# Performance work log

Hardware: AMD Instinct MI355X
Metric: run time of the kernel (lower is better)

Reference implementation:

```python
import jax, jax.numpy as jnp
import numpy as np

B, P, T = 32, 196, 32           # batch, num pixels (14*14), seq_len
E, H, A, V = 512, 512, 256, 30000  # embed, hidden, attention, vocab
FEAT = 2048

def _ln(x, g, b, eps=1e-5):
    m = jnp.mean(x, -1, keepdims=True)
    v = jnp.mean((x - m) ** 2, -1, keepdims=True)
    return (x - m) / jnp.sqrt(v + eps) * g + b

def setup_inputs() -> dict:
    key = jax.random.key(0)
    ks = iter(jax.random.split(key, 32))
    def rn(shape, s=0.05):
        return (jax.random.normal(next(ks), shape, dtype=jnp.float32) * s)
    inp = {
        'features': jax.random.normal(next(ks), (B, P, FEAT), dtype=jnp.float32),
        'captions': jax.random.randint(next(ks), (B, T), 0, V),
        # feature adapter Linear(2048->E) + LayerNorm
        'Wad': rn((E, FEAT)), 'bad': jnp.zeros((E,), jnp.float32),
        'g_ad': jnp.ones((E,), jnp.float32), 'b_ad': jnp.zeros((E,), jnp.float32),
        # additive attention
        'We': rn((A, E)), 'be': jnp.zeros((A,), jnp.float32),
        'Wd': rn((A, H)), 'bd': jnp.zeros((A,), jnp.float32),
        'Wf': rn((1, A)), 'bf': jnp.zeros((1,), jnp.float32),
        # embedding table (uniform(-0.1,0.1) as in torch init)
        'emb': jax.random.uniform(next(ks), (V, E), jnp.float32, -0.1, 0.1),
        # LSTM layer 0: input 2E, layer 1: input H; gates order i,f,g,o; forget bias 1
        'W_ih0': rn((4 * H, 2 * E)), 'W_hh0': rn((4 * H, H)),
        'b_ih0': jnp.concatenate([jnp.zeros(H), jnp.ones(H), jnp.zeros(2 * H)]).astype(jnp.float32),
        'b_hh0': jnp.zeros((4 * H,), jnp.float32),
        'W_ih1': rn((4 * H, H)), 'W_hh1': rn((4 * H, H)),
        'b_ih1': jnp.concatenate([jnp.zeros(H), jnp.ones(H), jnp.zeros(2 * H)]).astype(jnp.float32),
        'b_hh1': jnp.zeros((4 * H,), jnp.float32),
        # output head
        'W1': rn((H // 2, H)), 'b1': jnp.zeros((H // 2,), jnp.float32),
        'g1': jnp.ones((H // 2,), jnp.float32), 'bb1': jnp.zeros((H // 2,), jnp.float32),
        'W2': rn((V, H // 2)), 'b2': jnp.zeros((V,), jnp.float32),
    }
    return inp

def reference(features, captions, Wad, bad, g_ad, b_ad, We, be, Wd, bd, Wf, bf,
              emb, W_ih0, W_hh0, b_ih0, b_hh0, W_ih1, W_hh1, b_ih1, b_hh1,
              W1, b1, g1, bb1, W2, b2):
    # feature adapter (dropout = identity in eval)
    enc = _ln(jax.nn.relu(features @ Wad.T + bad), g_ad, b_ad)   # [B,P,E]
    att1 = enc @ We.T + be                                        # [B,P,A] (same every step)
    embs = emb[captions]                                          # [B,T,E]

    def lstm_cell(x, h, c, Wih, Whh, bih, bhh):
        gates = x @ Wih.T + bih + h @ Whh.T + bhh                 # [B,4H]
        i, f, g, o = jnp.split(gates, 4, axis=1)
        c_n = jax.nn.sigmoid(f) * c + jax.nn.sigmoid(i) * jnp.tanh(g)
        h_n = jax.nn.sigmoid(o) * jnp.tanh(c_n)
        return h_n, c_n

    def step(carry, emb_t):
        h, c = carry                                              # each [2,B,H]
        # additive attention against top-layer hidden state
        att2 = h[1] @ Wd.T + bd                                   # [B,A]
        e = (jax.nn.relu(att1 + att2[:, None, :]) @ Wf.T + bf)[..., 0]  # [B,P]
        alpha = jax.nn.softmax(e, axis=1)                         # (max-subtract is folded in)
        ctx = jnp.einsum('bp,bpe->be', alpha, enc)                # [B,E]
        x = jnp.concatenate([emb_t, ctx], axis=1)                 # [B,2E]
        h0, c0 = lstm_cell(x,  h[0], c[0], W_ih0, W_hh0, b_ih0, b_hh0)
        h1, c1 = lstm_cell(h0, h[1], c[1], W_ih1, W_hh1, b_ih1, b_hh1)
        out = jax.nn.relu(_ln(h1 @ W1.T + b1, g1, bb1))
        out = jnp.clip(out @ W2.T + b2, -10.0, 10.0)              # [B,V]
        return (jnp.stack([h0, h1]), jnp.stack([c0, c1])), out

    h0 = jnp.zeros((2, B, H), jnp.float32)
    c0 = jnp.zeros((2, B, H), jnp.float32)
    _, outs = jax.lax.scan(step, (h0, c0), jnp.swapaxes(embs, 0, 1))
    return jnp.swapaxes(outs, 0, 1)                               # [B,T,V]
```

## Files before the change

### kernel.cpp

```cpp
#include <hip/hip_runtime.h>

#define B_ 32
#define P_ 196
#define T_ 32
#define E_ 512
#define H_ 512
#define A_ 256
#define V_ 30000
#define FEAT_ 2048

typedef unsigned short u16;
typedef __attribute__((ext_vector_type(8))) short bf16x8;
typedef __attribute__((ext_vector_type(4))) float fx4;

#define MFMA16 __builtin_amdgcn_mfma_f32_16x16x32_bf16

__device__ __forceinline__ u16 f2b(float f){
  unsigned u = __builtin_bit_cast(unsigned, f);
  u += 0x7FFFu + ((u >> 16) & 1u);
  return (u16)(u >> 16);
}
__device__ __forceinline__ float b2f(u16 h){
  unsigned u = ((unsigned)h) << 16;
  return __builtin_bit_cast(float, u);
}
__device__ __forceinline__ float sigm(float x){ return 1.f/(1.f + __expf(-x)); }

__global__ void k_convert(const float* __restrict__ src, u16* __restrict__ dst, int n8){
  int i = blockIdx.x*256 + threadIdx.x;
  if (i >= n8) return;
  const float4* s = (const float4*)src + (size_t)i*2;
  float4 a = s[0], b = s[1];
  ushort4* d = (ushort4*)dst + (size_t)i*2;
  d[0] = make_ushort4(f2b(a.x), f2b(a.y), f2b(a.z), f2b(a.w));
  d[1] = make_ushort4(f2b(b.x), f2b(b.y), f2b(b.z), f2b(b.w));
}

__global__ void k_gather(const float* __restrict__ emb, const int* __restrict__ cap,
                         u16* __restrict__ dst){
  int r = blockIdx.x, l = threadIdx.x;
  int t = r >> 5, b = r & 31;
  int c = cap[b*T_ + t];
  const float4* s = (const float4*)(emb + (size_t)c*E_) + l*2;
  float4 a = s[0], bb = s[1];
  ushort4* d = (ushort4*)(dst + (size_t)r*E_) + l*2;
  d[0] = make_ushort4(f2b(a.x), f2b(a.y), f2b(a.z), f2b(a.w));
  d[1] = make_ushort4(f2b(bb.x), f2b(bb.y), f2b(bb.z), f2b(bb.w));
}

__global__ void k_pack_wd2(const float* __restrict__ Wd, unsigned* __restrict__ dst){
  int i = blockIdx.x*256 + threadIdx.x;
  if (i >= 256*256) return;
  int n = i & 255, kp = i >> 8;
  unsigned lo = f2b(Wd[n*512 + 2*kp]);
  unsigned hi = f2b(Wd[n*512 + 2*kp + 1]);
  dst[i] = lo | (hi << 16);
}

__global__ void k_pack_g0(const float* __restrict__ Wih, const float* __restrict__ Whh,
                          u16* __restrict__ dst){
  int eid = blockIdx.x*256 + threadIdx.x;
  if (eid >= 6144*512) return;
  int j = eid & 7, l = (eid >> 3) & 63, frag = eid >> 9;
  int ks = frag % 12; int rest = frag / 12;
  int kw = rest & 3, q = (rest >> 2) & 3, s = rest >> 4;
  int n = q*512 + s*16 + (l & 15);
  int k = kw*384 + ks*32 + ((l >> 4) << 3) + j;
  float v = (k < 1024) ? Wih[(size_t)n*1024 + k] : Whh[(size_t)n*512 + (k - 1024)];
  dst[eid] = f2b(v);
}

__global__ void k_pack_w1p(const float* __restrict__ Wih, const float* __restrict__ Whh,
                           u16* __restrict__ dst){
  int eid = blockIdx.x*256 + threadIdx.x;
  if (eid >= 32*128*512) return;
  int j = eid & 7, l = (eid >> 3) & 63, f = eid >> 9;
  int nf = f & 127, s = f >> 7;
  int np = nf*16 + (l & 15);
  int k = ((l >> 4) << 3) + j;
  int orig = ((np >> 4) & 3)*512 + (np >> 6)*16 + (np & 15);
  float v = (k < 16) ? Wih[(size_t)orig*512 + s*16 + k]
                     : Whh[(size_t)orig*512 + s*16 + (k - 16)];
  dst[eid] = f2b(v);
}

__global__ void k_bias_pack(const float* __restrict__ bih, const float* __restrict__ bhh,
                            float* __restrict__ dst){
  int n = blockIdx.x*256 + threadIdx.x;
  if (n >= 2048) return;
  int c = n & 15, q = (n >> 4) & 3, s = n >> 6;
  int orig = q*512 + s*16 + c;
  dst[n] = bih[orig] + bhh[orig];
}

template<int MODE, int BM, int BN>
__launch_bounds__(256)
__global__ void k_gemm(const u16* __restrict__ A, const u16* __restrict__ W,
                       const float* __restrict__ bias, float* __restrict__ outF,
                       u16* __restrict__ outB, int M, int N, int K){
  constexpr int NI = BN/32, MI = BM/32;
  __shared__ __align__(16) u16 As[BM][40];
  __shared__ __align__(16) u16 Bs[BN][40];
  int tid = threadIdx.x;
  int l = tid & 63, w = tid >> 6;
  int wr = w >> 1, wc = w & 1;
  int m0 = blockIdx.y * BM, n0 = blockIdx.x * BN;
  fx4 acc[MI][NI];
  #pragma unroll
  for (int i=0;i<MI;i++)
    #pragma unroll
    for (int j=0;j<NI;j++) acc[i][j] = (fx4){0.f,0.f,0.f,0.f};
  int r = tid >> 2, seg = tid & 3;
  int lr = l & 15, lg = l >> 4;
  for (int k0 = 0; k0 < K; k0 += 32){
    #pragma unroll
    for (int pa=0; pa<BM/64; pa++)
      *(uint4*)&As[r+pa*64][seg*8] = *(const uint4*)(A + (size_t)(m0+r+pa*64)*K + k0 + seg*8);
    uint4 z = {0u,0u,0u,0u};
    #pragma unroll
    for (int pb=0; pb<BN/64; pb++){
      int rb = n0 + r + pb*64;
      *(uint4*)&Bs[r+pb*64][seg*8] = (rb < N) ? *(const uint4*)(W + (size_t)rb*K + k0 + seg*8) : z;
    }
    __syncthreads();
    bf16x8 av[MI], bv[NI];
    #pragma unroll
    for (int mi=0; mi<MI; mi++) av[mi] = *(const bf16x8*)&As[wr*(BM/2) + mi*16 + lr][lg*8];
    #pragma unroll
    for (int ni=0; ni<NI; ni++) bv[ni] = *(const bf16x8*)&Bs[wc*(BN/2) + ni*16 + lr][lg*8];
    #pragma unroll
    for (int mi=0; mi<MI; mi++)
      #pragma unroll
      for (int ni=0; ni<NI; ni++)
        acc[mi][ni] = MFMA16(av[mi], bv[ni], acc[mi][ni], 0, 0, 0);
    __syncthreads();
  }
  #pragma unroll
  for (int mi=0; mi<MI; mi++)
    #pragma unroll
    for (int ni=0; ni<NI; ni++){
      int col = n0 + wc*(BN/2) + ni*16 + lr;
      if (col >= N) continue;
      float bvs = bias[col];
      #pragma unroll
      for (int reg=0; reg<4; reg++){
        int rowm = m0 + wr*(BM/2) + mi*16 + lg*4 + reg;
        float v = acc[mi][ni][reg] + bvs;
        if (MODE == 0){ v = fmaxf(v, 0.f); outB[(size_t)rowm*N + col] = f2b(v); }
        else if (MODE == 1){ outB[(size_t)rowm*N + col] = f2b(v); }
        else if (MODE == 2){ outF[(size_t)rowm*N + col] = v; }
        else {
          v = fminf(fmaxf(v, -10.f), 10.f);
          outF[(size_t)rowm*V_ + col] = v;
        }
      }
    }
}

__global__ void k_ln1(const u16* __restrict__ pre, const float* __restrict__ g,
                      const float* __restrict__ bt, u16* __restrict__ enc){
  int row = blockIdx.x; int l = threadIdx.x;
  bf16x8 vv = *(const bf16x8*)(pre + (size_t)row*E_ + l*8);
  float x[8]; float s = 0.f;
  #pragma unroll
  for (int i=0;i<8;i++){ x[i] = b2f((u16)vv[i]); s += x[i]; }
  #pragma unroll
  for (int off=32; off; off>>=1) s += __shfl_xor(s, off, 64);
  float mean = s * (1.f/512.f);
  float vs = 0.f;
  #pragma unroll
  for (int i=0;i<8;i++){ float d = x[i]-mean; vs += d*d; }
  #pragma unroll
  for (int off=32; off; off>>=1) vs += __shfl_xor(vs, off, 64);
  float inv = rsqrtf(vs*(1.f/512.f) + 1e-5f);
  int c0 = l*8;
  u16 o[8];
  #pragma unroll
  for (int i=0;i<8;i++) o[i] = f2b((x[i]-mean)*inv*g[c0+i] + bt[c0+i]);
  ushort4* d = (ushort4*)(enc + (size_t)row*E_ + c0);
  d[0] = make_ushort4(o[0],o[1],o[2],o[3]);
  d[1] = make_ushort4(o[4],o[5],o[6],o[7]);
}

__global__ void k_ln2(const float* __restrict__ pre1, const float* __restrict__ g,
                      const float* __restrict__ bb, u16* __restrict__ hid){
  int row = blockIdx.x; int l = threadIdx.x;
  float4 v = *(const float4*)(pre1 + (size_t)row*256 + l*4);
  float x[4] = {v.x, v.y, v.z, v.w};
  float s = x[0]+x[1]+x[2]+x[3];
  #pragma unroll
  for (int off=32; off; off>>=1) s += __shfl_xor(s, off, 64);
  float mean = s * (1.f/256.f);
  float vs = 0.f;
  #pragma unroll
  for (int i=0;i<4;i++){ float d = x[i]-mean; vs += d*d; }
  #pragma unroll
  for (int off=32; off; off>>=1) vs += __shfl_xor(vs, off, 64);
  float inv = rsqrtf(vs*(1.f/256.f) + 1e-5f);
  int c0 = l*4;
  u16 o[4];
  #pragma unroll
  for (int i=0;i<4;i++) o[i] = f2b(fmaxf((x[i]-mean)*inv*g[c0+i] + bb[c0+i], 0.f));
  *(ushort4*)(hid + (size_t)row*256 + c0) = make_ushort4(o[0],o[1],o[2],o[3]);
}

__launch_bounds__(1024)
__global__ void k_ly(const float* __restrict__ part1, const float* __restrict__ bias1p,
                     float* __restrict__ c1buf, u16* __restrict__ h1all,
                     const unsigned* __restrict__ Wd2, const float* __restrict__ bd,
                     const u16* __restrict__ att1b, const u16* __restrict__ enc16,
                     const float* __restrict__ Wf, const float* __restrict__ bfp,
                     const u16* __restrict__ embs, u16* __restrict__ xh0cur, int t){
  int b = blockIdx.x, tid = threadIdx.x;
  int l = tid & 63, wid = tid >> 6;
  __shared__ float g1s[2048];
  __shared__ float h1s[512];
  __shared__ float a2p[4][256];
  __shared__ float a2[256], ev[256], red[8], wfv[256], bdv[256];
  __shared__ float cb[4][256][2];
  if (tid < 256){ wfv[tid] = Wf[tid]; bdv[tid] = bd[tid]; }
  float bf0 = bfp[0];

  if (t > 0){
    float acc0 = bias1p[tid], acc1 = bias1p[tid + 1024];
    #pragma unroll 4
    for (int s2=0; s2<32; ++s2){
      const float* pp = part1 + ((size_t)(s2*32 + b))*2048;
      acc0 += pp[tid];
      acc1 += pp[tid + 1024];
    }
    g1s[tid] = acc0; g1s[tid + 1024] = acc1;
    __syncthreads();
    if (tid < 512){
      int h = tid, s4 = h >> 4, c = h & 15, base = s4*64 + c;
      float gi = g1s[base], gf = g1s[base+16], gg = g1s[base+32], go = g1s[base+48];
      float cold = c1buf[b*512 + h];
      float cn = sigm(gf)*cold + sigm(gi)*tanhf(gg);
      c1buf[b*512 + h] = cn;
      float hn = sigm(go)*tanhf(cn);
      h1s[h] = hn;
      h1all[((size_t)b*T_ + (t-1))*512 + h] = f2b(hn);
    }
  } else {
    if (tid < 512) h1s[tid] = 0.f;
  }
  __syncthreads();
  if (t >= T_) return;

  {
    int n = tid & 255, kq = tid >> 8;
    float acc = 0.f;
    const unsigned* wp = Wd2 + (size_t)kq*64*256 + n;
    #pragma unroll 8
    for (int kp2 = 0; kp2 < 64; ++kp2){
      unsigned wv = wp[(size_t)kp2*256];
      int k0 = (kq*64 + kp2)*2;
      acc += h1s[k0]   * b2f((u16)(wv & 0xFFFFu))
           + h1s[k0+1] * b2f((u16)(wv >> 16));
    }
    a2p[kq][n] = acc;
  }
  __syncthreads();
  if (tid < 256) a2[tid] = a2p[0][tid] + a2p[1][tid] + a2p[2][tid] + a2p[3][tid] + bdv[tid];
  __syncthreads();
  for (int pi = 0; pi < 13; ++pi){
    int p = pi*16 + wid;
    if (p < P_){
      ushort4 av4 = *(const ushort4*)(att1b + (size_t)(b*P_ + p)*A_ + l*4);
      int j0 = l*4;
      float sum = fmaxf(b2f(av4.x)+a2[j0],  0.f)*wfv[j0]
                + fmaxf(b2f(av4.y)+a2[j0+1],0.f)*wfv[j0+1]
                + fmaxf(b2f(av4.z)+a2[j0+2],0.f)*wfv[j0+2]
                + fmaxf(b2f(av4.w)+a2[j0+3],0.f)*wfv[j0+3];
      #pragma unroll
      for (int off=32; off; off>>=1) sum += __shfl_xor(sum, off, 64);
      if (l == 0) ev[p] = sum + bf0;
    }
  }
  __syncthreads();
  if (tid < 256){
    float v = (tid < P_) ? ev[tid] : -1e30f;
    float m = v;
    #pragma unroll
    for (int off=32; off; off>>=1) m = fmaxf(m, __shfl_xor(m, off, 64));
    if (l == 0) red[wid] = m;
  }
  __syncthreads();
  float mg = fmaxf(fmaxf(red[0],red[1]), fmaxf(red[2],red[3]));
  if (tid < 256){
    float ex = (tid < P_) ? __expf(ev[tid] - mg) : 0.f;
    float ss = ex;
    #pragma unroll
    for (int off=32; off; off>>=1) ss += __shfl_xor(ss, off, 64);
    if (l == 0) red[4+wid] = ss;
    ev[tid] = ex;
  }
  __syncthreads();
  float inv = 1.f/(red[4]+red[5]+red[6]+red[7]);
  {
    int j = tid & 255, pq = tid >> 8;
    float A0 = 0.f, A1 = 0.f;
    const unsigned* ep = (const unsigned*)enc16 + ((size_t)b*P_ + pq*49)*256 + j;
    #pragma unroll 7
    for (int pi = 0; pi < 49; ++pi){
      unsigned vv = ep[(size_t)pi*256];
      float al = ev[pq*49 + pi];
      A0 += al * b2f((u16)(vv & 0xFFFFu));
      A1 += al * b2f((u16)(vv >> 16));
    }
    cb[pq][j][0] = A0; cb[pq][j][1] = A1;
  }
  __syncthreads();
  if (tid < 256){
    float c0 = (cb[0][tid][0]+cb[1][tid][0]+cb[2][tid][0]+cb[3][tid][0]) * inv;
    float c1 = (cb[0][tid][1]+cb[1][tid][1]+cb[2][tid][1]+cb[3][tid][1]) * inv;
    unsigned o = (unsigned)f2b(c0) | (((unsigned)f2b(c1)) << 16);
    *((unsigned*)(xh0cur + (size_t)b*1536 + 512) + tid) = o;
    ((unsigned*)(xh0cur + (size_t)b*1536))[tid] =
        ((const unsigned*)(embs + (size_t)(t*32+b)*E_))[tid];
  }
}

__launch_bounds__(1024)
__global__ void k_lx(const u16* __restrict__ xh0cur, u16* __restrict__ xh0nxt,
                     const u16* __restrict__ Wg0pk, const float* __restrict__ bias0p,
                     const u16* __restrict__ W1ppk, const u16* __restrict__ h1all,
                     float* __restrict__ c0buf, float* __restrict__ part1, int t){
  __shared__ float part[16][32][16];
  __shared__ float gsum[4][32][16];
  __shared__ __align__(16) u16 As[32][40];
  int tid = threadIdx.x, s = blockIdx.x;
  int l = tid & 63, kw = tid >> 6, lr = l & 15, lg = l >> 4;

  bf16x8 a[2][3];
  #pragma unroll
  for (int mi=0;mi<2;mi++)
    #pragma unroll
    for (int ks=0;ks<3;ks++)
      a[mi][ks] = *(const bf16x8*)(xh0cur + (size_t)(mi*16+lr)*1536 + kw*96 + ks*32 + lg*8);
  for (int q=0;q<4;q++){
    fx4 acc0 = (fx4){0,0,0,0}, acc1 = (fx4){0,0,0,0};
    const u16* wp = Wg0pk + (size_t)(((s*4+q)*4 + (kw>>2))*12 + (kw&3)*3)*512 + l*8;
    #pragma unroll
    for (int ks=0;ks<3;ks++){
      bf16x8 bf8 = *(const bf16x8*)(wp + ks*512);
      acc0 = MFMA16(a[0][ks], bf8, acc0, 0,0,0);
      acc1 = MFMA16(a[1][ks], bf8, acc1, 0,0,0);
    }
    #pragma unroll
    for (int reg=0;reg<4;reg++){
      part[kw][lg*4+reg][lr]    = acc0[reg];
      part[kw][16+lg*4+reg][lr] = acc1[reg];
    }
    __syncthreads();
    if (tid < 512){
      int bb = tid >> 4, c = tid & 15;
      float g = bias0p[s*64 + q*16 + c];
      #pragma unroll
      for (int kw2=0; kw2<16; ++kw2) g += part[kw2][bb][c];
      gsum[q][bb][c] = g;
    }
    __syncthreads();
  }
  if (tid < 256){
    int bb = tid >> 3, kk = (tid & 7)*2;
    unsigned hv = 0;
    if (t > 0) hv = *(const unsigned*)(h1all + ((size_t)bb*T_ + (t-1))*512 + s*16 + kk);
    *(unsigned*)&As[bb][16+kk] = hv;
  }
  if (tid < 512){
    int bb = tid >> 4, c = tid & 15;
    int h = s*16 + c;
    float gi = gsum[0][bb][c], gf = gsum[1][bb][c], gg = gsum[2][bb][c], go = gsum[3][bb][c];
    float cold = c0buf[bb*512 + h];
    float cn = sigm(gf)*cold + sigm(gi)*tanhf(gg);
    c0buf[bb*512 + h] = cn;
    u16 hb = f2b(sigm(go)*tanhf(cn));
    xh0nxt[(size_t)bb*1536 + 1024 + h] = hb;
    As[bb][c] = hb;
  }
  __syncthreads();
  bf16x8 pa0 = *(const bf16x8*)&As[lr][lg*8];
  bf16x8 pa1 = *(const bf16x8*)&As[16+lr][lg*8];
  #pragma unroll 2
  for (int i=0;i<8;i++){
    int nf = kw*8 + i;
    bf16x8 bf8 = *(const bf16x8*)(W1ppk + (size_t)(s*128 + nf)*512 + l*8);
    fx4 A0 = MFMA16(pa0, bf8, (fx4){0,0,0,0}, 0,0,0);
    fx4 A1 = MFMA16(pa1, bf8, (fx4){0,0,0,0}, 0,0,0);
    float* o = part1 + ((size_t)s*32)*2048 + nf*16 + lr;
    #pragma unroll
    for (int reg=0;reg<4;reg++){
      o[(size_t)(lg*4+reg)*2048]    = A0[reg];
      o[(size_t)(16+lg*4+reg)*2048] = A1[reg];
    }
  }
}

extern "C" void kernel_launch(void* const* d_in, const int* in_sizes, int n_in,
                              void* d_out, int out_size, void* d_ws, size_t ws_size,
                              hipStream_t stream){
  (void)in_sizes; (void)n_in; (void)out_size; (void)ws_size;
  const float* features = (const float*)d_in[0];
  const int*   captions = (const int*)d_in[1];
  const float* Wad  = (const float*)d_in[2];
  const float* bad  = (const float*)d_in[3];
  const float* g_ad = (const float*)d_in[4];
  const float* b_ad = (const float*)d_in[5];
  const float* We   = (const float*)d_in[6];
  const float* be   = (const float*)d_in[7];
  const float* Wd   = (const float*)d_in[8];
  const float* bd   = (const float*)d_in[9];
  const float* Wf   = (const float*)d_in[10];
  const float* bfp  = (const float*)d_in[11];
  const float* emb  = (const float*)d_in[12];
  const float* W_ih0 = (const float*)d_in[13];
  const float* W_hh0 = (const float*)d_in[14];
  const float* b_ih0 = (const float*)d_in[15];
  const float* b_hh0 = (const float*)d_in[16];
  const float* W_ih1 = (const float*)d_in[17];
  const float* W_hh1 = (const float*)d_in[18];
  const float* b_ih1 = (const float*)d_in[19];
  const float* b_hh1 = (const float*)d_in[20];
  const float* W1  = (const float*)d_in[21];
  const float* b1  = (const float*)d_in[22];
  const float* g1  = (const float*)d_in[23];
  const float* bb1 = (const float*)d_in[24];
  const float* W2  = (const float*)d_in[25];
  const float* b2  = (const float*)d_in[26];
  float* out = (float*)d_out;

  char* wsb = (char*)d_ws;
  size_t off = 0;
  auto alloc = [&](size_t bytes)->char*{
    char* p = wsb + off; off += (bytes + 255) & ~(size_t)255; return p;
  };
  u16* fb16    = (u16*)alloc((size_t)6272*2048*2);
  u16* Wad16   = (u16*)alloc((size_t)512*2048*2);
  u16* We16    = (u16*)alloc((size_t)256*512*2);
  u16* W1_16   = (u16*)alloc((size_t)256*512*2);
  u16* W2_16   = (u16*)alloc((size_t)30000*256*2);
  unsigned* Wd2 = (unsigned*)alloc((size_t)256*256*4);
  u16* Wg0pk   = (u16*)alloc((size_t)2048*1536*2);
  u16* W1ppk   = (u16*)alloc((size_t)32*128*512*2);
  float* bias0p = (float*)alloc(2048*4);
  float* bias1p = (float*)alloc(2048*4);
  u16* embs16  = (u16*)alloc((size_t)1024*512*2);
  u16* pre16   = (u16*)alloc((size_t)6272*512*2);
  u16* enc16   = (u16*)alloc((size_t)6272*512*2);
  u16* att1_16 = (u16*)alloc((size_t)6272*256*2);
  u16* xh0     = (u16*)alloc((size_t)2*32*1536*2);
  float* c0buf = (float*)alloc(32*512*4);
  float* c1buf = (float*)alloc(32*512*4);
  float* part1 = (float*)alloc((size_t)32*32*2048*4);
  u16* h1all16 = (u16*)alloc((size_t)1024*512*2);
  float* pre1  = (float*)alloc((size_t)1024*256*4);
  u16* hid16   = (u16*)alloc((size_t)1024*256*2);

  auto cdiv = [](int a, int b){ return (a+b-1)/b; };

  hipMemsetAsync(xh0, 0, 196608 + 65536 + 65536, stream);

  k_convert<<<cdiv(6272*2048/8,256),256,0,stream>>>(features, fb16, 6272*2048/8);
  k_convert<<<cdiv(512*2048/8,256),256,0,stream>>>(Wad, Wad16, 512*2048/8);
  k_convert<<<cdiv(256*512/8,256),256,0,stream>>>(We, We16, 256*512/8);
  k_convert<<<cdiv(256*512/8,256),256,0,stream>>>(W1, W1_16, 256*512/8);
  k_convert<<<cdiv(30000*256/8,256),256,0,stream>>>(W2, W2_16, 30000*256/8);
  k_pack_wd2<<<cdiv(256*256,256),256,0,stream>>>(Wd, Wd2);
  k_pack_g0<<<cdiv(6144*512,256),256,0,stream>>>(W_ih0, W_hh0, Wg0pk);
  k_pack_w1p<<<cdiv(32*128*512,256),256,0,stream>>>(W_ih1, W_hh1, W1ppk);
  k_bias_pack<<<8,256,0,stream>>>(b_ih0, b_hh0, bias0p);
  k_bias_pack<<<8,256,0,stream>>>(b_ih1, b_hh1, bias1p);
  k_gather<<<1024,64,0,stream>>>(emb, captions, embs16);

  k_gemm<0,64,64><<<dim3(8,98),256,0,stream>>>(fb16, Wad16, bad, nullptr, pre16, 6272, 512, 2048);
  k_ln1<<<6272,64,0,stream>>>(pre16, g_ad, b_ad, enc16);
  k_gemm<1,64,64><<<dim3(4,98),256,0,stream>>>(enc16, We16, be, nullptr, att1_16, 6272, 256, 512);

  u16* xb[2] = { xh0, xh0 + 32*1536 };
  for (int t = 0; t < T_; ++t){
    k_ly<<<32,1024,0,stream>>>(part1, bias1p, c1buf, h1all16, Wd2, bd,
                               att1_16, enc16, Wf, bfp, embs16, xb[t&1], t);
    k_lx<<<32,1024,0,stream>>>(xb[t&1], xb[1-(t&1)], Wg0pk, bias0p,
                               W1ppk, h1all16, c0buf, part1, t);
  }
  k_ly<<<32,1024,0,stream>>>(part1, bias1p, c1buf, h1all16, Wd2, bd,
                             att1_16, enc16, Wf, bfp, embs16, xb[0], T_);

  k_gemm<2,64,64><<<dim3(4,16),256,0,stream>>>(h1all16, W1_16, b1, pre1, nullptr, 1024, 256, 512);
  k_ln2<<<1024,64,0,stream>>>(pre1, g1, bb1, hid16);
  k_gemm<3,64,128><<<dim3(235,16),256,0,stream>>>(hid16, W2_16, b2, out, nullptr, 1024, 30000, 256);
}
```

Baseline: 1.395 ms.

## Stage GEMM epilogue through LDS, vectorize partial sums, use LDS atomics in LSTM step

```diff
diff --git a/kernel.cpp b/kernel.cpp
--- a/kernel.cpp
+++ b/kernel.cpp
@@ -101,6 +101,7 @@
   constexpr int NI = BN/32, MI = BM/32;
   __shared__ __align__(16) u16 As[BM][40];
   __shared__ __align__(16) u16 Bs[BN][40];
+  __shared__ __align__(16) float Cs[BM][BN+4];
   int tid = threadIdx.x;
   int l = tid & 63, w = tid >> 6;
   int wr = w >> 1, wc = w & 1;
@@ -139,22 +140,48 @@
   for (int mi=0; mi<MI; mi++)
     #pragma unroll
     for (int ni=0; ni<NI; ni++){
-      int col = n0 + wc*(BN/2) + ni*16 + lr;
-      if (col >= N) continue;
-      float bvs = bias[col];
+      int col = wc*(BN/2) + ni*16 + lr;
+      float bvs = (n0 + col < N) ? bias[n0 + col] : 0.f;
       #pragma unroll
       for (int reg=0; reg<4; reg++){
-        int rowm = m0 + wr*(BM/2) + mi*16 + lg*4 + reg;
+        int rowl = wr*(BM/2) + mi*16 + lg*4 + reg;
         float v = acc[mi][ni][reg] + bvs;
-        if (MODE == 0){ v = fmaxf(v, 0.f); outB[(size_t)rowm*N + col] = f2b(v); }
-        else if (MODE == 1){ outB[(size_t)rowm*N + col] = f2b(v); }
-        else if (MODE == 2){ outF[(size_t)rowm*N + col] = v; }
-        else {
-          v = fminf(fmaxf(v, -10.f), 10.f);
-          outF[(size_t)rowm*V_ + col] = v;
-        }
+        if (MODE == 0) v = fmaxf(v, 0.f);
+        if (MODE == 3) v = fminf(fmaxf(v, -10.f), 10.f);
+        Cs[rowl][col] = v;
       }
     }
+  __syncthreads();
+  if (MODE >= 2){
+    constexpr int F4 = BN/4;
+    int ldo = (MODE == 3) ? V_ : N;
+    #pragma unroll
+    for (int it=0; it<BM*F4/256; ++it){
+      int idx = it*256 + tid;
+      int rr = idx / F4, cc = (idx % F4)*4;
+      int col = n0 + cc;
+      if (col < N){
+        float4 val = { Cs[rr][cc], Cs[rr][cc+1], Cs[rr][cc+2], Cs[rr][cc+3] };
+        *(float4*)(outF + (size_t)(m0+rr)*ldo + col) = val;
+      }
+    }
+  } else {
+    constexpr int F8 = BN/8;
+    #pragma unroll
+    for (int it=0; it<BM*F8/256; ++it){
+      int idx = it*256 + tid;
+      int rr = idx / F8, cc = (idx % F8)*8;
+      int col = n0 + cc;
+      if (col < N){
+        ushort4 o0 = make_ushort4(f2b(Cs[rr][cc+0]), f2b(Cs[rr][cc+1]),
+                                  f2b(Cs[rr][cc+2]), f2b(Cs[rr][cc+3]));
+        ushort4 o1 = make_ushort4(f2b(Cs[rr][cc+4]), f2b(Cs[rr][cc+5]),
+                                  f2b(Cs[rr][cc+6]), f2b(Cs[rr][cc+7]));
+        ushort4* d = (ushort4*)(outB + (size_t)(m0+rr)*N + col);
+        d[0] = o0; d[1] = o1;
+      }
+    }
+  }
 }
 
 __global__ void k_ln1(const u16* __restrict__ pre, const float* __restrict__ g,
@@ -213,23 +240,38 @@
                      const u16* __restrict__ embs, u16* __restrict__ xh0cur, int t){
   int b = blockIdx.x, tid = threadIdx.x;
   int l = tid & 63, wid = tid >> 6;
+  __shared__ fx4  s1[2][512];
   __shared__ float g1s[2048];
   __shared__ float h1s[512];
   __shared__ float a2p[4][256];
   __shared__ float a2[256], ev[256], red[8], wfv[256], bdv[256];
   __shared__ float cb[4][256][2];
+  ushort4 av4p[13];
+  #pragma unroll
+  for (int pi=0; pi<13; ++pi){
+    int p = pi*16 + wid;
+    av4p[pi] = (p < P_) ? *(const ushort4*)(att1b + (size_t)(b*P_ + p)*A_ + l*4)
+                        : make_ushort4(0,0,0,0);
+  }
   if (tid < 256){ wfv[tid] = Wf[tid]; bdv[tid] = bd[tid]; }
   float bf0 = bfp[0];
 
   if (t > 0){
-    float acc0 = bias1p[tid], acc1 = bias1p[tid + 1024];
+    int grp = tid >> 9, j4 = tid & 511;
+    fx4 accv = (fx4){0.f,0.f,0.f,0.f};
     #pragma unroll 4
-    for (int s2=0; s2<32; ++s2){
-      const float* pp = part1 + ((size_t)(s2*32 + b))*2048;
-      acc0 += pp[tid];
-      acc1 += pp[tid + 1024];
-    }
-    g1s[tid] = acc0; g1s[tid + 1024] = acc1;
+    for (int s2=0; s2<16; ++s2){
+      const float* pp = part1 + ((size_t)((grp*16+s2)*32 + b))*2048 + j4*4;
+      accv += *(const fx4*)pp;
+    }
+    s1[grp][j4] = accv;
+    __syncthreads();
+    {
+      int e = tid;
+      g1s[e]      = s1[0][e>>2][e&3]           + s1[1][e>>2][e&3]           + bias1p[e];
+      int e2 = tid + 1024;
+      g1s[e2]     = s1[0][e2>>2][e2&3]         + s1[1][e2>>2][e2&3]         + bias1p[e2];
+    }
     __syncthreads();
     if (tid < 512){
       int h = tid, s4 = h >> 4, c = h & 15, base = s4*64 + c;
@@ -263,10 +305,11 @@
   __syncthreads();
   if (tid < 256) a2[tid] = a2p[0][tid] + a2p[1][tid] + a2p[2][tid] + a2p[3][tid] + bdv[tid];
   __syncthreads();
+  #pragma unroll
   for (int pi = 0; pi < 13; ++pi){
     int p = pi*16 + wid;
     if (p < P_){
-      ushort4 av4 = *(const ushort4*)(att1b + (size_t)(b*P_ + p)*A_ + l*4);
+      ushort4 av4 = av4p[pi];
       int j0 = l*4;
       float sum = fmaxf(b2f(av4.x)+a2[j0],  0.f)*wfv[j0]
                 + fmaxf(b2f(av4.y)+a2[j0+1],0.f)*wfv[j0+1]
@@ -326,8 +369,7 @@
                      const u16* __restrict__ Wg0pk, const float* __restrict__ bias0p,
                      const u16* __restrict__ W1ppk, const u16* __restrict__ h1all,
                      float* __restrict__ c0buf, float* __restrict__ part1, int t){
-  __shared__ float part[16][32][16];
-  __shared__ float gsum[4][32][16];
+  __shared__ float gacc[4][32][16];
   __shared__ __align__(16) u16 As[32][40];
   int tid = threadIdx.x, s = blockIdx.x;
   int l = tid & 63, kw = tid >> 6, lr = l & 15, lg = l >> 4;
@@ -338,29 +380,13 @@
     #pragma unroll
     for (int ks=0;ks<3;ks++)
       a[mi][ks] = *(const bf16x8*)(xh0cur + (size_t)(mi*16+lr)*1536 + kw*96 + ks*32 + lg*8);
-  for (int q=0;q<4;q++){
-    fx4 acc0 = (fx4){0,0,0,0}, acc1 = (fx4){0,0,0,0};
-    const u16* wp = Wg0pk + (size_t)(((s*4+q)*4 + (kw>>2))*12 + (kw&3)*3)*512 + l*8;
-    #pragma unroll
-    for (int ks=0;ks<3;ks++){
-      bf16x8 bf8 = *(const bf16x8*)(wp + ks*512);
-      acc0 = MFMA16(a[0][ks], bf8, acc0, 0,0,0);
-      acc1 = MFMA16(a[1][ks], bf8, acc1, 0,0,0);
-    }
-    #pragma unroll
-    for (int reg=0;reg<4;reg++){
-      part[kw][lg*4+reg][lr]    = acc0[reg];
-      part[kw][16+lg*4+reg][lr] = acc1[reg];
-    }
-    __syncthreads();
-    if (tid < 512){
-      int bb = tid >> 4, c = tid & 15;
-      float g = bias0p[s*64 + q*16 + c];
-      #pragma unroll
-      for (int kw2=0; kw2<16; ++kw2) g += part[kw2][bb][c];
-      gsum[q][bb][c] = g;
-    }
-    __syncthreads();
+
+  {
+    float* gf = (float*)gacc;
+    int e = tid;
+    gf[e]        = ((e>>4)&31) < 32 ? bias0p[s*64 + (e>>9)*16 + (e&15)]    : 0.f;
+    int e2 = tid + 1024;
+    gf[e2]       = bias0p[s*64 + (e2>>9)*16 + (e2&15)];
   }
   if (tid < 256){
     int bb = tid >> 3, kk = (tid & 7)*2;
@@ -368,10 +394,30 @@
     if (t > 0) hv = *(const unsigned*)(h1all + ((size_t)bb*T_ + (t-1))*512 + s*16 + kk);
     *(unsigned*)&As[bb][16+kk] = hv;
   }
+  __syncthreads();
+
+  #pragma unroll
+  for (int q=0;q<4;q++){
+    fx4 acc0 = (fx4){0,0,0,0}, acc1 = (fx4){0,0,0,0};
+    const u16* wp = Wg0pk + (size_t)(((s*4+q)*4 + (kw>>2))*12 + (kw&3)*3)*512 + l*8;
+    #pragma unroll
+    for (int ks=0;ks<3;ks++){
+      bf16x8 bf8 = *(const bf16x8*)(wp + ks*512);
+      acc0 = MFMA16(a[0][ks], bf8, acc0, 0,0,0);
+      acc1 = MFMA16(a[1][ks], bf8, acc1, 0,0,0);
+    }
+    #pragma unroll
+    for (int reg=0;reg<4;reg++){
+      atomicAdd(&gacc[q][lg*4+reg][lr],    acc0[reg]);
+      atomicAdd(&gacc[q][16+lg*4+reg][lr], acc1[reg]);
+    }
+  }
+  __syncthreads();
+
   if (tid < 512){
     int bb = tid >> 4, c = tid & 15;
     int h = s*16 + c;
-    float gi = gsum[0][bb][c], gf = gsum[1][bb][c], gg = gsum[2][bb][c], go = gsum[3][bb][c];
+    float gi = gacc[0][bb][c], gf = gacc[1][bb][c], gg = gacc[2][bb][c], go = gacc[3][bb][c];
     float cold = c0buf[bb*512 + h];
     float cn = sigm(gf)*cold + sigm(gi)*tanhf(gg);
     c0buf[bb*512 + h] = cn;
@@ -380,6 +426,7 @@
     As[bb][c] = hb;
   }
   __syncthreads();
+
   bf16x8 pa0 = *(const bf16x8*)&As[lr][lg*8];
   bf16x8 pa1 = *(const bf16x8*)&As[16+lr][lg*8];
   #pragma unroll 2
```

Result: slower. 2.514 ms (+80.2%).

## Fuse feature conversion into adapter GEMM and rebuild output head kernels

Applied to the files above, without the earlier changes.

```diff
diff --git a/kernel.cpp b/kernel.cpp
--- a/kernel.cpp
+++ b/kernel.cpp
@@ -93,14 +93,27 @@
   dst[n] = bih[orig] + bhh[orig];
 }
 
-template<int MODE, int BM, int BN>
+__global__ void k_pack_w2(const float* __restrict__ W2f, u16* __restrict__ W2pk){
+  int i = blockIdx.x*256 + threadIdx.x;
+  if (i >= 960000) return;
+  int l = i & 63, kc = (i >> 6) & 7, nf = i >> 9;
+  int row = nf*16 + (l & 15);
+  int col = kc*32 + (l >> 4)*8;
+  const float4* s = (const float4*)(W2f + (size_t)row*256 + col);
+  float4 a = s[0], b = s[1];
+  ushort4* d = (ushort4*)(W2pk + (size_t)i*8);
+  d[0] = make_ushort4(f2b(a.x), f2b(a.y), f2b(a.z), f2b(a.w));
+  d[1] = make_ushort4(f2b(b.x), f2b(b.y), f2b(b.z), f2b(b.w));
+}
+
+template<int MODE, int BM, int BN, int KS>
 __launch_bounds__(256)
 __global__ void k_gemm(const u16* __restrict__ A, const u16* __restrict__ W,
-                       const float* __restrict__ bias, float* __restrict__ outF,
-                       u16* __restrict__ outB, int M, int N, int K){
-  constexpr int NI = BN/32, MI = BM/32;
-  __shared__ __align__(16) u16 As[BM][40];
-  __shared__ __align__(16) u16 Bs[BN][40];
+                       const float* __restrict__ bias, u16* __restrict__ outB,
+                       int M, int N, int K){
+  constexpr int NI = BN/32, MI = BM/32, SEGS = KS/8;
+  __shared__ __align__(16) u16 As[BM][KS+8];
+  __shared__ __align__(16) u16 Bs[BN][KS+8];
   int tid = threadIdx.x;
   int l = tid & 63, w = tid >> 6;
   int wr = w >> 1, wc = w & 1;
@@ -110,29 +123,34 @@
   for (int i=0;i<MI;i++)
     #pragma unroll
     for (int j=0;j<NI;j++) acc[i][j] = (fx4){0.f,0.f,0.f,0.f};
-  int r = tid >> 2, seg = tid & 3;
   int lr = l & 15, lg = l >> 4;
-  for (int k0 = 0; k0 < K; k0 += 32){
-    #pragma unroll
-    for (int pa=0; pa<BM/64; pa++)
-      *(uint4*)&As[r+pa*64][seg*8] = *(const uint4*)(A + (size_t)(m0+r+pa*64)*K + k0 + seg*8);
+  for (int k0 = 0; k0 < K; k0 += KS){
+    #pragma unroll
+    for (int it=0; it<BM*SEGS/256; ++it){
+      int flat = it*256 + tid, rr = flat/SEGS, cs = (flat%SEGS)*8;
+      *(uint4*)&As[rr][cs] = *(const uint4*)(A + (size_t)(m0+rr)*K + k0 + cs);
+    }
     uint4 z = {0u,0u,0u,0u};
     #pragma unroll
-    for (int pb=0; pb<BN/64; pb++){
-      int rb = n0 + r + pb*64;
-      *(uint4*)&Bs[r+pb*64][seg*8] = (rb < N) ? *(const uint4*)(W + (size_t)rb*K + k0 + seg*8) : z;
-    }
-    __syncthreads();
-    bf16x8 av[MI], bv[NI];
-    #pragma unroll
-    for (int mi=0; mi<MI; mi++) av[mi] = *(const bf16x8*)&As[wr*(BM/2) + mi*16 + lr][lg*8];
-    #pragma unroll
-    for (int ni=0; ni<NI; ni++) bv[ni] = *(const bf16x8*)&Bs[wc*(BN/2) + ni*16 + lr][lg*8];
-    #pragma unroll
-    for (int mi=0; mi<MI; mi++)
-      #pragma unroll
-      for (int ni=0; ni<NI; ni++)
-        acc[mi][ni] = MFMA16(av[mi], bv[ni], acc[mi][ni], 0, 0, 0);
+    for (int it=0; it<BN*SEGS/256; ++it){
+      int flat = it*256 + tid, rr = flat/SEGS, cs = (flat%SEGS)*8;
+      int rb = n0 + rr;
+      *(uint4*)&Bs[rr][cs] = (rb < N) ? *(const uint4*)(W + (size_t)rb*K + k0 + cs) : z;
+    }
+    __syncthreads();
+    #pragma unroll
+    for (int kk=0; kk<KS/32; ++kk){
+      bf16x8 av[MI], bv[NI];
+      #pragma unroll
+      for (int mi=0; mi<MI; mi++) av[mi] = *(const bf16x8*)&As[wr*(BM/2) + mi*16 + lr][kk*32 + lg*8];
+      #pragma unroll
+      for (int ni=0; ni<NI; ni++) bv[ni] = *(const bf16x8*)&Bs[wc*(BN/2) + ni*16 + lr][kk*32 + lg*8];
+      #pragma unroll
+      for (int mi=0; mi<MI; mi++)
+        #pragma unroll
+        for (int ni=0; ni<NI; ni++)
+          acc[mi][ni] = MFMA16(av[mi], bv[ni], acc[mi][ni], 0, 0, 0);
+    }
     __syncthreads();
   }
   #pragma unroll
@@ -146,13 +164,71 @@
       for (int reg=0; reg<4; reg++){
         int rowm = m0 + wr*(BM/2) + mi*16 + lg*4 + reg;
         float v = acc[mi][ni][reg] + bvs;
-        if (MODE == 0){ v = fmaxf(v, 0.f); outB[(size_t)rowm*N + col] = f2b(v); }
-        else if (MODE == 1){ outB[(size_t)rowm*N + col] = f2b(v); }
-        else if (MODE == 2){ outF[(size_t)rowm*N + col] = v; }
-        else {
-          v = fminf(fmaxf(v, -10.f), 10.f);
-          outF[(size_t)rowm*V_ + col] = v;
-        }
+        if (MODE == 0) v = fmaxf(v, 0.f);
+        outB[(size_t)rowm*N + col] = f2b(v);
+      }
+    }
+}
+
+template<int BM, int BN, int KS>
+__launch_bounds__(256)
+__global__ void k_gemmF(const float* __restrict__ A, const u16* __restrict__ W,
+                        const float* __restrict__ bias, u16* __restrict__ outB,
+                        int M, int N, int K){
+  constexpr int NI = BN/32, MI = BM/32, SEGS = KS/8;
+  __shared__ __align__(16) u16 As[BM][KS+8];
+  __shared__ __align__(16) u16 Bs[BN][KS+8];
+  int tid = threadIdx.x;
+  int l = tid & 63, w = tid >> 6;
+  int wr = w >> 1, wc = w & 1;
+  int m0 = blockIdx.y * BM, n0 = blockIdx.x * BN;
+  fx4 acc[MI][NI];
+  #pragma unroll
+  for (int i=0;i<MI;i++)
+    #pragma unroll
+    for (int j=0;j<NI;j++) acc[i][j] = (fx4){0.f,0.f,0.f,0.f};
+  int lr = l & 15, lg = l >> 4;
+  for (int k0 = 0; k0 < K; k0 += KS){
+    #pragma unroll
+    for (int it=0; it<BM*SEGS/256; ++it){
+      int flat = it*256 + tid, rr = flat/SEGS, cs = (flat%SEGS)*8;
+      const float4* s = (const float4*)(A + (size_t)(m0+rr)*K + k0 + cs);
+      float4 a0 = s[0], a1 = s[1];
+      *(ushort4*)&As[rr][cs]   = make_ushort4(f2b(a0.x), f2b(a0.y), f2b(a0.z), f2b(a0.w));
+      *(ushort4*)&As[rr][cs+4] = make_ushort4(f2b(a1.x), f2b(a1.y), f2b(a1.z), f2b(a1.w));
+    }
+    #pragma unroll
+    for (int it=0; it<BN*SEGS/256; ++it){
+      int flat = it*256 + tid, rr = flat/SEGS, cs = (flat%SEGS)*8;
+      *(uint4*)&Bs[rr][cs] = *(const uint4*)(W + (size_t)(n0+rr)*K + k0 + cs);
+    }
+    __syncthreads();
+    #pragma unroll
+    for (int kk=0; kk<KS/32; ++kk){
+      bf16x8 av[MI], bv[NI];
+      #pragma unroll
+      for (int mi=0; mi<MI; mi++) av[mi] = *(const bf16x8*)&As[wr*(BM/2) + mi*16 + lr][kk*32 + lg*8];
+      #pragma unroll
+      for (int ni=0; ni<NI; ni++) bv[ni] = *(const bf16x8*)&Bs[wc*(BN/2) + ni*16 + lr][kk*32 + lg*8];
+      #pragma unroll
+      for (int mi=0; mi<MI; mi++)
+        #pragma unroll
+        for (int ni=0; ni<NI; ni++)
+          acc[mi][ni] = MFMA16(av[mi], bv[ni], acc[mi][ni], 0, 0, 0);
+    }
+    __syncthreads();
+  }
+  #pragma unroll
+  for (int mi=0; mi<MI; mi++)
+    #pragma unroll
+    for (int ni=0; ni<NI; ni++){
+      int col = n0 + wc*(BN/2) + ni*16 + lr;
+      float bvs = bias[col];
+      #pragma unroll
+      for (int reg=0; reg<4; reg++){
+        int rowm = m0 + wr*(BM/2) + mi*16 + lg*4 + reg;
+        float v = fmaxf(acc[mi][ni][reg] + bvs, 0.f);
+        outB[(size_t)rowm*N + col] = f2b(v);
       }
     }
 }
@@ -182,26 +258,137 @@
   d[1] = make_ushort4(o[4],o[5],o[6],o[7]);
 }
 
-__global__ void k_ln2(const float* __restrict__ pre1, const float* __restrict__ g,
-                      const float* __restrict__ bb, u16* __restrict__ hid){
-  int row = blockIdx.x; int l = threadIdx.x;
-  float4 v = *(const float4*)(pre1 + (size_t)row*256 + l*4);
-  float x[4] = {v.x, v.y, v.z, v.w};
-  float s = x[0]+x[1]+x[2]+x[3];
-  #pragma unroll
-  for (int off=32; off; off>>=1) s += __shfl_xor(s, off, 64);
-  float mean = s * (1.f/256.f);
-  float vs = 0.f;
-  #pragma unroll
-  for (int i=0;i<4;i++){ float d = x[i]-mean; vs += d*d; }
-  #pragma unroll
-  for (int off=32; off; off>>=1) vs += __shfl_xor(vs, off, 64);
-  float inv = rsqrtf(vs*(1.f/256.f) + 1e-5f);
-  int c0 = l*4;
-  u16 o[4];
-  #pragma unroll
-  for (int i=0;i<4;i++) o[i] = f2b(fmaxf((x[i]-mean)*inv*g[c0+i] + bb[c0+i], 0.f));
-  *(ushort4*)(hid + (size_t)row*256 + c0) = make_ushort4(o[0],o[1],o[2],o[3]);
+__device__ __forceinline__ void w1ln_block(const u16* __restrict__ h1all,
+    const u16* __restrict__ W1, const float* __restrict__ b1,
+    const float* __restrict__ g1v, const float* __restrict__ bb1,
+    u16* __restrict__ hid, int u, int tid, float* red2, float* mv){
+  int l = tid & 63, w = tid >> 6, lr = l & 15, lg = l >> 4;
+  fx4 acc[2] = {{0,0,0,0},{0,0,0,0}};
+  for (int k0 = 0; k0 < 512; k0 += 32){
+    bf16x8 bv  = *(const bf16x8*)(W1 + (size_t)(w*16+lr)*512 + k0 + lg*8);
+    bf16x8 av0 = *(const bf16x8*)(h1all + ((size_t)lr*T_ + u)*512 + k0 + lg*8);
+    bf16x8 av1 = *(const bf16x8*)(h1all + ((size_t)(16+lr)*T_ + u)*512 + k0 + lg*8);
+    acc[0] = MFMA16(av0, bv, acc[0], 0,0,0);
+    acc[1] = MFMA16(av1, bv, acc[1], 0,0,0);
+  }
+  int col = w*16 + lr;
+  float bc = b1[col];
+  float val[2][4], s1[2][4], s2[2][4];
+  #pragma unroll
+  for (int mi=0;mi<2;mi++)
+    #pragma unroll
+    for (int reg=0;reg<4;reg++){
+      float v = acc[mi][reg] + bc;
+      val[mi][reg] = v; s1[mi][reg] = v; s2[mi][reg] = v*v;
+    }
+  #pragma unroll
+  for (int off=1; off<16; off<<=1){
+    #pragma unroll
+    for (int mi=0;mi<2;mi++)
+      #pragma unroll
+      for (int reg=0;reg<4;reg++){
+        s1[mi][reg] += __shfl_xor(s1[mi][reg], off, 64);
+        s2[mi][reg] += __shfl_xor(s2[mi][reg], off, 64);
+      }
+  }
+  if (lr == 0){
+    #pragma unroll
+    for (int mi=0;mi<2;mi++)
+      #pragma unroll
+      for (int reg=0;reg<4;reg++){
+        int row = mi*16 + lg*4 + reg;
+        red2[(0*16 + w)*32 + row] = s1[mi][reg];
+        red2[(16   + w)*32 + row] = s2[mi][reg];
+      }
+  }
+  __syncthreads();
+  if (tid < 64){
+    int which = tid >> 5, row = tid & 31;
+    float s = 0.f;
+    #pragma unroll
+    for (int ww=0; ww<16; ++ww) s += red2[(which*16 + ww)*32 + row];
+    mv[which*32 + row] = s;
+  }
+  __syncthreads();
+  #pragma unroll
+  for (int mi=0;mi<2;mi++)
+    #pragma unroll
+    for (int reg=0;reg<4;reg++){
+      int row = mi*16 + lg*4 + reg;
+      float mean = mv[row] * (1.f/256.f);
+      float var  = mv[32+row] * (1.f/256.f) - mean*mean;
+      float inv  = rsqrtf(var + 1e-5f);
+      float o = fmaxf((val[mi][reg]-mean)*inv*g1v[col] + bb1[col], 0.f);
+      hid[((size_t)u*32 + row)*256 + col] = f2b(o);
+    }
+}
+
+__launch_bounds__(1024)
+__global__ void k_w1(const u16* __restrict__ h1all, const u16* __restrict__ W1_16,
+                     const float* __restrict__ b1, const float* __restrict__ g1v,
+                     const float* __restrict__ bb1, u16* __restrict__ hid16){
+  __shared__ float red2[1024];
+  __shared__ float mv[64];
+  w1ln_block(h1all, W1_16, b1, g1v, bb1, hid16, blockIdx.x, threadIdx.x, red2, mv);
+}
+
+__launch_bounds__(1024)
+__global__ void k_head(const u16* __restrict__ hid, const u16* __restrict__ W2pk,
+                       const float* __restrict__ b2, float* __restrict__ out){
+  __shared__ __align__(16) union { u16 hA[32][264]; float Cs[32][260]; } S;
+  int c = blockIdx.x, uh = blockIdx.y, tid = threadIdx.x;
+  int l = tid & 63, w = tid >> 6, lr = l & 15, lg = l >> 4;
+  int nf = c*16 + w;
+  bool valid = nf < 1875;
+  bf16x8 bw[8];
+  if (valid){
+    const u16* wp = W2pk + (size_t)nf*4096 + l*8;
+    #pragma unroll
+    for (int k0=0;k0<8;k0++) bw[k0] = *(const bf16x8*)(wp + k0*512);
+  }
+  int srow = tid >> 5, scc = (tid & 31)*8;
+  int col0 = c*256 + scc;
+  float bb[8];
+  #pragma unroll
+  for (int j=0;j<8;j++) bb[j] = (col0 + j < V_) ? b2[col0 + j] : 0.f;
+
+  for (int ui=0; ui<16; ++ui){
+    int u = uh*16 + ui;
+    { int arow = tid >> 5, ak = (tid & 31)*8;
+      *(uint4*)&S.hA[arow][ak] = *(const uint4*)(hid + ((size_t)u*32 + arow)*256 + ak); }
+    __syncthreads();
+    fx4 acc0 = {0,0,0,0}, acc1 = {0,0,0,0};
+    if (valid){
+      #pragma unroll
+      for (int k0=0;k0<8;k0++){
+        bf16x8 av0 = *(const bf16x8*)&S.hA[lr][k0*32 + lg*8];
+        bf16x8 av1 = *(const bf16x8*)&S.hA[16+lr][k0*32 + lg*8];
+        acc0 = MFMA16(av0, bw[k0], acc0, 0,0,0);
+        acc1 = MFMA16(av1, bw[k0], acc1, 0,0,0);
+      }
+    }
+    __syncthreads();
+    #pragma unroll
+    for (int reg=0; reg<4; ++reg){
+      S.Cs[lg*4+reg][w*16+lr]    = acc0[reg];
+      S.Cs[16+lg*4+reg][w*16+lr] = acc1[reg];
+    }
+    __syncthreads();
+    if (col0 + 8 <= V_){
+      float4 v0, v1;
+      v0.x = fminf(fmaxf(S.Cs[srow][scc+0] + bb[0], -10.f), 10.f);
+      v0.y = fminf(fmaxf(S.Cs[srow][scc+1] + bb[1], -10.f), 10.f);
+      v0.z = fminf(fmaxf(S.Cs[srow][scc+2] + bb[2], -10.f), 10.f);
+      v0.w = fminf(fmaxf(S.Cs[srow][scc+3] + bb[3], -10.f), 10.f);
+      v1.x = fminf(fmaxf(S.Cs[srow][scc+4] + bb[4], -10.f), 10.f);
+      v1.y = fminf(fmaxf(S.Cs[srow][scc+5] + bb[5], -10.f), 10.f);
+      v1.z = fminf(fmaxf(S.Cs[srow][scc+6] + bb[6], -10.f), 10.f);
+      v1.w = fminf(fmaxf(S.Cs[srow][scc+7] + bb[7], -10.f), 10.f);
+      float* o = out + ((size_t)srow*T_ + u)*V_ + col0;
+      *(float4*)o = v0; *(float4*)(o+4) = v1;
+    }
+    __syncthreads();
+  }
 }
 
 __launch_bounds__(1024)
@@ -435,11 +622,10 @@
   auto alloc = [&](size_t bytes)->char*{
     char* p = wsb + off; off += (bytes + 255) & ~(size_t)255; return p;
   };
-  u16* fb16    = (u16*)alloc((size_t)6272*2048*2);
   u16* Wad16   = (u16*)alloc((size_t)512*2048*2);
   u16* We16    = (u16*)alloc((size_t)256*512*2);
   u16* W1_16   = (u16*)alloc((size_t)256*512*2);
-  u16* W2_16   = (u16*)alloc((size_t)30000*256*2);
+  u16* W2pk    = (u16*)alloc((size_t)1875*8*512*2);
   unsigned* Wd2 = (unsigned*)alloc((size_t)256*256*4);
   u16* Wg0pk   = (u16*)alloc((size_t)2048*1536*2);
   u16* W1ppk   = (u16*)alloc((size_t)32*128*512*2);
@@ -454,18 +640,16 @@
   float* c1buf = (float*)alloc(32*512*4);
   float* part1 = (float*)alloc((size_t)32*32*2048*4);
   u16* h1all16 = (u16*)alloc((size_t)1024*512*2);
-  float* pre1  = (float*)alloc((size_t)1024*256*4);
   u16* hid16   = (u16*)alloc((size_t)1024*256*2);
 
   auto cdiv = [](int a, int b){ return (a+b-1)/b; };
 
   hipMemsetAsync(xh0, 0, 196608 + 65536 + 65536, stream);
 
-  k_convert<<<cdiv(6272*2048/8,256),256,0,stream>>>(features, fb16, 6272*2048/8);
   k_convert<<<cdiv(512*2048/8,256),256,0,stream>>>(Wad, Wad16, 512*2048/8);
   k_convert<<<cdiv(256*512/8,256),256,0,stream>>>(We, We16, 256*512/8);
   k_convert<<<cdiv(256*512/8,256),256,0,stream>>>(W1, W1_16, 256*512/8);
-  k_convert<<<cdiv(30000*256/8,256),256,0,stream>>>(W2, W2_16, 30000*256/8);
+  k_pack_w2<<<cdiv(960000,256),256,0,stream>>>(W2, W2pk);
   k_pack_wd2<<<cdiv(256*256,256),256,0,stream>>>(Wd, Wd2);
   k_pack_g0<<<cdiv(6144*512,256),256,0,stream>>>(W_ih0, W_hh0, Wg0pk);
   k_pack_w1p<<<cdiv(32*128*512,256),256,0,stream>>>(W_ih1, W_hh1, W1ppk);
@@ -473,9 +657,9 @@
   k_bias_pack<<<8,256,0,stream>>>(b_ih1, b_hh1, bias1p);
   k_gather<<<1024,64,0,stream>>>(emb, captions, embs16);
 
-  k_gemm<0,64,64><<<dim3(8,98),256,0,stream>>>(fb16, Wad16, bad, nullptr, pre16, 6272, 512, 2048);
+  k_gemmF<64,64,64><<<dim3(8,98),256,0,stream>>>(features, Wad16, bad, pre16, 6272, 512, 2048);
   k_ln1<<<6272,64,0,stream>>>(pre16, g_ad, b_ad, enc16);
-  k_gemm<1,64,64><<<dim3(4,98),256,0,stream>>>(enc16, We16, be, nullptr, att1_16, 6272, 256, 512);
+  k_gemm<1,64,64,64><<<dim3(4,98),256,0,stream>>>(enc16, We16, be, att1_16, 6272, 256, 512);
 
   u16* xb[2] = { xh0, xh0 + 32*1536 };
   for (int t = 0; t < T_; ++t){
@@ -487,7 +671,6 @@
   k_ly<<<32,1024,0,stream>>>(part1, bias1p, c1buf, h1all16, Wd2, bd,
                              att1_16, enc16, Wf, bfp, embs16, xb[0], T_);
 
-  k_gemm<2,64,64><<<dim3(4,16),256,0,stream>>>(h1all16, W1_16, b1, pre1, nullptr, 1024, 256, 512);
-  k_ln2<<<1024,64,0,stream>>>(pre1, g1, bb1, hid16);
-  k_gemm<3,64,128><<<dim3(235,16),256,0,stream>>>(hid16, W2_16, b2, out, nullptr, 1024, 30000, 256);
-}
+  k_w1<<<32,1024,0,stream>>>(h1all16, W1_16, b1, g1, bb1, hid16);
+  k_head<<<dim3(118,2),1024,0,stream>>>(hid16, W2pk, b2, out);
+}
```

Measured after the change: 1.367 ms (median of 3 runs). 1.02x faster.
